# Kernel optimization log

Measured on AMD Instinct MI355X. Metric: run time of the kernel, lower is better.

## Reference

```python
import jax, jax.numpy as jnp
import numpy as np
import math

B, N, DIM = 16, 1024, 384
DEPTH, HEADS, DH = 6, 6, 64
INNER = HEADS * DH          # 384
MLP = 1536
LN_EPS = 1e-5


def setup_inputs() -> dict:
    key = jax.random.key(0)
    ks = jax.random.split(key, 7)
    s = 0.02
    x = jax.random.normal(ks[0], (B, N, DIM), dtype=jnp.float32)
    ln1_g = jnp.ones((DEPTH, DIM), jnp.float32)
    ln1_b = jnp.zeros((DEPTH, DIM), jnp.float32)
    qkv_w = jax.random.normal(ks[1], (DEPTH, DIM, 3 * INNER), jnp.float32) * s
    temp = jnp.full((DEPTH,), math.log(DH ** -0.5), jnp.float32)
    out_w = jax.random.normal(ks[2], (DEPTH, INNER, DIM), jnp.float32) * s
    out_b = jnp.zeros((DEPTH, DIM), jnp.float32)
    ln2_g = jnp.ones((DEPTH, DIM), jnp.float32)
    ln2_b = jnp.zeros((DEPTH, DIM), jnp.float32)
    ff_w1 = jax.random.normal(ks[3], (DEPTH, DIM, MLP), jnp.float32) * s
    ff_b1 = jnp.zeros((DEPTH, MLP), jnp.float32)
    ff_w2 = jax.random.normal(ks[4], (DEPTH, MLP, DIM), jnp.float32) * s
    ff_b2 = jnp.zeros((DEPTH, DIM), jnp.float32)
    return dict(x=x, ln1_g=ln1_g, ln1_b=ln1_b, qkv_w=qkv_w, temp=temp,
                out_w=out_w, out_b=out_b, ln2_g=ln2_g, ln2_b=ln2_b,
                ff_w1=ff_w1, ff_b1=ff_b1, ff_w2=ff_w2, ff_b2=ff_b2)


def _ln(x, g, b):
    m = jnp.mean(x, axis=-1, keepdims=True)
    v = jnp.var(x, axis=-1, keepdims=True)
    return (x - m) * jax.lax.rsqrt(v + LN_EPS) * g + b


def reference(x, ln1_g, ln1_b, qkv_w, temp, out_w, out_b,
              ln2_g, ln2_b, ff_w1, ff_b1, ff_w2, ff_b2):
    neg = -jnp.finfo(x.dtype).max
    eye = jnp.eye(N, dtype=bool)

    def step(x, p):
        g1, b1, wqkv, t, wo, bo, g2, b2, w1, bb1, w2, bb2 = p
        # --- PreNorm + LSA attention ---
        h = _ln(x, g1, b1)
        qkv = h @ wqkv                              # [B, N, 3*INNER]
        q, k, v = jnp.split(qkv, 3, axis=-1)
        split_heads = lambda a: a.reshape(B, N, HEADS, DH).transpose(0, 2, 1, 3)
        q, k, v = split_heads(q), split_heads(k), split_heads(v)
        dots = jnp.einsum('bhnd,bhmd->bhnm', q, k) * jnp.exp(t)
        dots = jnp.where(eye, neg, dots)            # mask diagonal (LSA)
        attn = jax.nn.softmax(dots, axis=-1)
        o = jnp.einsum('bhnm,bhmd->bhnd', attn, v)
        o = o.transpose(0, 2, 1, 3).reshape(B, N, INNER)
        x = x + o @ wo + bo
        # --- PreNorm + FeedForward (exact GELU) ---
        h2 = _ln(x, g2, b2)
        ff = jax.nn.gelu(h2 @ w1 + bb1, approximate=False) @ w2 + bb2
        x = x + ff
        return x, None

    params = (ln1_g, ln1_b, qkv_w, temp, out_w, out_b,
              ln2_g, ln2_b, ff_w1, ff_b1, ff_w2, ff_b2)
    x, _ = jax.lax.scan(step, x, params)
    return x
```

## Files before the change

### kernel.cpp

```cpp
#include <hip/hip_runtime.h>
#include <hip/hip_bf16.h>
#include <math.h>

#define B_     16
#define NTOK   1024
#define DIM_   384
#define DEPTH_ 6
#define HEADS_ 6
#define DH_    64
#define MLP_   1536
#define MTOT   (B_ * NTOK)
#define NBH    (B_ * HEADS_)

typedef unsigned short u16;
typedef unsigned int u32;
typedef short short8 __attribute__((ext_vector_type(8)));
typedef float f32x4 __attribute__((ext_vector_type(4)));

static __device__ __forceinline__ u16 f2b(float f) {
    __hip_bfloat16 h = __float2bfloat16(f);
    return *reinterpret_cast<u16*>(&h);
}

#define GLOAD_LDS16(gp, lp)                                                     \
    __builtin_amdgcn_global_load_lds(                                           \
        (const __attribute__((address_space(1))) void*)(gp),                    \
        (__attribute__((address_space(3))) void*)(lp), 16, 0, 0)

__launch_bounds__(256)
__global__ void transpose_w_kernel(const float* __restrict__ W, u16* __restrict__ WT,
                                   int K, int N) {
    const int layer = blockIdx.z;
    W  += (size_t)layer * K * N;
    WT += (size_t)layer * K * N;
    __shared__ u16 tile[64 * 72];
    const int t = threadIdx.x;
    const int k0 = blockIdx.x * 64, n0 = blockIdx.y * 64;
    const int row = t >> 2, cs = (t & 3) * 16;
    const float4* src = reinterpret_cast<const float4*>(W + (size_t)(k0 + row) * N + n0 + cs);
#pragma unroll
    for (int i = 0; i < 4; i++) {
        float4 f = src[i];
        tile[row * 72 + cs + i * 4 + 0] = f2b(f.x);
        tile[row * 72 + cs + i * 4 + 1] = f2b(f.y);
        tile[row * 72 + cs + i * 4 + 2] = f2b(f.z);
        tile[row * 72 + cs + i * 4 + 3] = f2b(f.w);
    }
    __syncthreads();
    const int nrow = row, ks = cs;
    u16 vals[16] __attribute__((aligned(16)));
#pragma unroll
    for (int e = 0; e < 16; e++) vals[e] = tile[(ks + e) * 72 + nrow];
    u16* dst = WT + (size_t)(n0 + nrow) * K + k0 + ks;
    *reinterpret_cast<short8*>(dst)     = *reinterpret_cast<short8*>(&vals[0]);
    *reinterpret_cast<short8*>(dst + 8) = *reinterpret_cast<short8*>(&vals[8]);
}

__launch_bounds__(256)
__global__ void ln_kernel(const float* __restrict__ x, const float* __restrict__ g,
                          const float* __restrict__ b, u16* __restrict__ h) {
    const int tok  = blockIdx.x * 4 + (threadIdx.x >> 6);
    const int lane = threadIdx.x & 63;
    const float* xr = x + (size_t)tok * DIM_;
    float v[6];
    float s = 0.f;
#pragma unroll
    for (int i = 0; i < 6; i++) { v[i] = xr[lane + i * 64]; s += v[i]; }
#pragma unroll
    for (int m = 1; m < 64; m <<= 1) s += __shfl_xor(s, m);
    const float mean = s * (1.f / 384.f);
    float qs = 0.f;
#pragma unroll
    for (int i = 0; i < 6; i++) { float d = v[i] - mean; qs += d * d; }
#pragma unroll
    for (int m = 1; m < 64; m <<= 1) qs += __shfl_xor(qs, m);
    const float inv = rsqrtf(qs * (1.f / 384.f) + 1e-5f);
    u16* hr = h + (size_t)tok * DIM_;
#pragma unroll
    for (int i = 0; i < 6; i++) {
        const int c = lane + i * 64;
        hr[c] = f2b((v[i] - mean) * inv * g[c] + b[c]);
    }
}

enum { EPI_QKV = 0, EPI_RES = 1, EPI_GELU = 2 };

template <int EPI>
__launch_bounds__(256)
__global__ void gemm_kernel(const u16* __restrict__ A, const u16* __restrict__ BT, int K,
                            const float* __restrict__ bias, const float* __restrict__ resid,
                            float* __restrict__ outf, u16* __restrict__ outb, int ldc,
                            u16* __restrict__ qkv_base) {
    __shared__ u16 As[128 * 32];
    __shared__ u16 Bs[128 * 32];
    const int t = threadIdx.x;
    const int lane = t & 63, w = t >> 6;
    const int wm = w >> 1, wn = w & 1;
    const int m0 = blockIdx.x * 128, n0 = blockIdx.y * 128;

    f32x4 acc[4][4] = {};

    const int c0 = w * 2, c1 = w * 2 + 1;
    const int seg = (lane & 3) * 8;
    const u16* agp0 = A  + (size_t)(m0 + c0 * 16 + (lane >> 2)) * K + seg;
    const u16* agp1 = A  + (size_t)(m0 + c1 * 16 + (lane >> 2)) * K + seg;
    const u16* bgp0 = BT + (size_t)(n0 + c0 * 16 + (lane >> 2)) * K + seg;
    const u16* bgp1 = BT + (size_t)(n0 + c1 * 16 + (lane >> 2)) * K + seg;
    u16* asl0 = &As[c0 * 512];
    u16* asl1 = &As[c1 * 512];
    u16* bsl0 = &Bs[c0 * 512];
    u16* bsl1 = &Bs[c1 * 512];

    for (int kk = 0; kk < K; kk += 32) {
        __syncthreads();
        GLOAD_LDS16(agp0 + kk, asl0);
        GLOAD_LDS16(agp1 + kk, asl1);
        GLOAD_LDS16(bgp0 + kk, bsl0);
        GLOAD_LDS16(bgp1 + kk, bsl1);
        __syncthreads();
        short8 af[4], bf[4];
#pragma unroll
        for (int i = 0; i < 4; i++)
            af[i] = *reinterpret_cast<const short8*>(
                &As[(wm * 64 + i * 16 + (lane & 15)) * 32 + (lane >> 4) * 8]);
#pragma unroll
        for (int j = 0; j < 4; j++)
            bf[j] = *reinterpret_cast<const short8*>(
                &Bs[(wn * 64 + j * 16 + (lane & 15)) * 32 + (lane >> 4) * 8]);
#pragma unroll
        for (int i = 0; i < 4; i++)
#pragma unroll
            for (int j = 0; j < 4; j++)
                acc[i][j] = __builtin_amdgcn_mfma_f32_16x16x32_bf16(af[i], bf[j], acc[i][j], 0, 0, 0);
    }

    const int rbase = (lane >> 4) * 4;
    const int cb = lane & 15;
#pragma unroll
    for (int i = 0; i < 4; i++) {
#pragma unroll
        for (int j = 0; j < 4; j++) {
#pragma unroll
            for (int r = 0; r < 4; r++) {
                const int m = m0 + wm * 64 + i * 16 + rbase + r;
                const int c = n0 + wn * 64 + j * 16 + cb;
                const float val = acc[i][j][r];
                if constexpr (EPI == EPI_QKV) {
                    const int which = c / 384;
                    const int cc = c - which * 384;
                    const int head = cc >> 6, dh = cc & 63;
                    const int b = m >> 10, n = m & 1023;
                    qkv_base[(size_t)which * ((size_t)NBH * NTOK * DH_) +
                             ((size_t)((b * HEADS_ + head) * NTOK + n)) * DH_ + dh] = f2b(val);
                } else if constexpr (EPI == EPI_RES) {
                    outf[(size_t)m * ldc + c] = resid[(size_t)m * ldc + c] + bias[c] + val;
                } else {
                    const float xg = val + bias[c];
                    const float ge = 0.5f * xg * (1.0f + erff(xg * 0.70710678118f));
                    outb[(size_t)m * ldc + c] = f2b(ge);
                }
            }
        }
    }
}

__launch_bounds__(256)
__global__ void attn_kernel(const u16* __restrict__ q, const u16* __restrict__ k,
                            const u16* __restrict__ v, const float* __restrict__ temp,
                            u16* __restrict__ o) {
    __shared__ u16 Ks[64 * 72];
    __shared__ u16 Vt[64 * 88];
    __shared__ u16 Ps[4][16 * 80];
    const int t = threadIdx.x, lane = t & 63, w = t >> 6;
    const int g8 = lane >> 4, qi = lane & 15;
    const int bh = blockIdx.x, q0 = blockIdx.y * 64;
    const float scale = __expf(temp[0]);
    const size_t base = (size_t)bh * (NTOK * DH_);

    short8 bq[2];
#pragma unroll
    for (int s = 0; s < 2; s++)
        bq[s] = *reinterpret_cast<const short8*>(
            &q[base + (size_t)(q0 + w * 16 + qi) * 64 + s * 32 + g8 * 8]);

    float m_s = -3.0e38f, l_s = 0.f;
    f32x4 accO[4] = {};
    const int qglob = q0 + w * 16 + qi;

    for (int j0 = 0; j0 < NTOK; j0 += 64) {
        __syncthreads();
#pragma unroll
        for (int cc = 0; cc < 2; cc++) {
            const int idx = t + cc * 256;
            const int row = idx >> 3, ch = idx & 7;
            *reinterpret_cast<short8*>(&Ks[row * 72 + ch * 8]) =
                *reinterpret_cast<const short8*>(&k[base + (size_t)(j0 + row) * 64 + ch * 8]);
        }
#pragma unroll
        for (int cc = 0; cc < 2; cc++) {
            const int kv0 = w * 16 + cc * 8;
            u16 tmp[8] __attribute__((aligned(16)));
#pragma unroll
            for (int j = 0; j < 8; j++)
                tmp[j] = v[base + (size_t)(j0 + kv0 + j) * 64 + lane];
            *reinterpret_cast<short8*>(&Vt[lane * 88 + kv0]) = *reinterpret_cast<short8*>(&tmp[0]);
        }
        __syncthreads();

        f32x4 sf[4] = {};
#pragma unroll
        for (int c = 0; c < 4; c++)
#pragma unroll
            for (int s = 0; s < 2; s++) {
                short8 af = *reinterpret_cast<const short8*>(
                    &Ks[(c * 16 + qi) * 72 + s * 32 + g8 * 8]);
                sf[c] = __builtin_amdgcn_mfma_f32_16x16x32_bf16(af, bq[s], sf[c], 0, 0, 0);
            }

        float p[4][4];
        float vmax = -3.0e38f;
#pragma unroll
        for (int c = 0; c < 4; c++)
#pragma unroll
            for (int r = 0; r < 4; r++) {
                float sv = sf[c][r] * scale;
                const int kvg = j0 + c * 16 + g8 * 4 + r;
                if (kvg == qglob) sv = -1.0e30f;
                p[c][r] = sv;
                vmax = fmaxf(vmax, sv);
            }
        vmax = fmaxf(vmax, __shfl_xor(vmax, 16));
        vmax = fmaxf(vmax, __shfl_xor(vmax, 32));
        const float mnew = fmaxf(m_s, vmax);
        const float alpha = __expf(m_s - mnew);
        m_s = mnew;
        float tsum = 0.f;
#pragma unroll
        for (int c = 0; c < 4; c++)
#pragma unroll
            for (int r = 0; r < 4; r++) {
                const float pe = __expf(p[c][r] - mnew);
                p[c][r] = pe;
                tsum += pe;
            }
        tsum += __shfl_xor(tsum, 16);
        tsum += __shfl_xor(tsum, 32);
        l_s = l_s * alpha + tsum;

#pragma unroll
        for (int r = 0; r < 4; r++) {
            const float a_r = __shfl(alpha, g8 * 4 + r, 64);
#pragma unroll
            for (int g = 0; g < 4; g++) accO[g][r] *= a_r;
        }

#pragma unroll
        for (int c = 0; c < 4; c++) {
            u32 lo = (u32)f2b(p[c][0]) | ((u32)f2b(p[c][1]) << 16);
            u32 hi = (u32)f2b(p[c][2]) | ((u32)f2b(p[c][3]) << 16);
            uint2 pr; pr.x = lo; pr.y = hi;
            *reinterpret_cast<uint2*>(&Ps[w][qi * 80 + c * 16 + g8 * 4]) = pr;
        }

#pragma unroll
        for (int s = 0; s < 2; s++) {
            short8 ap = *reinterpret_cast<const short8*>(&Ps[w][qi * 80 + s * 32 + g8 * 8]);
#pragma unroll
            for (int g = 0; g < 4; g++) {
                short8 bv = *reinterpret_cast<const short8*>(
                    &Vt[(g * 16 + qi) * 88 + s * 32 + g8 * 8]);
                accO[g] = __builtin_amdgcn_mfma_f32_16x16x32_bf16(ap, bv, accO[g], 0, 0, 0);
            }
        }
    }

    const int bidx = bh / HEADS_, head = bh % HEADS_;
#pragma unroll
    for (int r = 0; r < 4; r++) {
        const float li = __shfl(l_s, g8 * 4 + r, 64);
        const float linv = 1.f / li;
        const int n = q0 + w * 16 + g8 * 4 + r;
#pragma unroll
        for (int g = 0; g < 4; g++) {
            const int dh = g * 16 + qi;
            o[((size_t)(bidx * NTOK + n)) * DIM_ + head * DH_ + dh] = f2b(accO[g][r] * linv);
        }
    }
}

extern "C" void kernel_launch(void* const* d_in, const int* in_sizes, int n_in,
                              void* d_out, int out_size, void* d_ws, size_t ws_size,
                              hipStream_t stream) {
    const float* x_in  = (const float*)d_in[0];
    const float* ln1_g = (const float*)d_in[1];
    const float* ln1_b = (const float*)d_in[2];
    const float* qkv_w = (const float*)d_in[3];
    const float* temp  = (const float*)d_in[4];
    const float* out_w = (const float*)d_in[5];
    const float* out_b = (const float*)d_in[6];
    const float* ln2_g = (const float*)d_in[7];
    const float* ln2_b = (const float*)d_in[8];
    const float* ff_w1 = (const float*)d_in[9];
    const float* ff_b1 = (const float*)d_in[10];
    const float* ff_w2 = (const float*)d_in[11];
    const float* ff_b2 = (const float*)d_in[12];

    char* ws = (char*)d_ws;
    size_t off = 0;
    auto alloc = [&](size_t bytes) -> void* {
        void* p = ws + off;
        off += (bytes + 255) & ~(size_t)255;
        return p;
    };
    u16* wt_qkv = (u16*)alloc((size_t)DEPTH_ * 1152 * 384 * 2);
    u16* wt_out = (u16*)alloc((size_t)DEPTH_ * 384 * 384 * 2);
    u16* wt_ff1 = (u16*)alloc((size_t)DEPTH_ * 1536 * 384 * 2);
    u16* wt_ff2 = (u16*)alloc((size_t)DEPTH_ * 384 * 1536 * 2);
    u16* H      = (u16*)alloc((size_t)MTOT * DIM_ * 2);
    u16* QKV    = (u16*)alloc((size_t)MTOT * MLP_ * 2);
    u16* MID    = QKV;

    float* X = (float*)d_out;

    hipMemcpyAsync(X, x_in, (size_t)MTOT * DIM_ * sizeof(float),
                   hipMemcpyDeviceToDevice, stream);

    transpose_w_kernel<<<dim3(6, 18, DEPTH_), 256, 0, stream>>>(qkv_w, wt_qkv, 384, 1152);
    transpose_w_kernel<<<dim3(6, 6, DEPTH_), 256, 0, stream>>>(out_w, wt_out, 384, 384);
    transpose_w_kernel<<<dim3(6, 24, DEPTH_), 256, 0, stream>>>(ff_w1, wt_ff1, 384, 1536);
    transpose_w_kernel<<<dim3(24, 6, DEPTH_), 256, 0, stream>>>(ff_w2, wt_ff2, 1536, 384);

    const size_t qkv_plane = (size_t)NBH * NTOK * DH_;

    for (int layer = 0; layer < DEPTH_; layer++) {
        ln_kernel<<<4096, 256, 0, stream>>>(X, ln1_g + layer * DIM_, ln1_b + layer * DIM_, H);
        gemm_kernel<EPI_QKV><<<dim3(128, 9), 256, 0, stream>>>(
            H, wt_qkv + (size_t)layer * 1152 * 384, 384,
            nullptr, nullptr, nullptr, nullptr, 0, QKV);
        attn_kernel<<<dim3(96, 16), 256, 0, stream>>>(
            QKV, QKV + qkv_plane, QKV + 2 * qkv_plane, temp + layer, H);
        gemm_kernel<EPI_RES><<<dim3(128, 3), 256, 0, stream>>>(
            H, wt_out + (size_t)layer * 384 * 384, 384,
            out_b + layer * DIM_, X, X, nullptr, DIM_, nullptr);
        ln_kernel<<<4096, 256, 0, stream>>>(X, ln2_g + layer * DIM_, ln2_b + layer * DIM_, H);
        gemm_kernel<EPI_GELU><<<dim3(128, 12), 256, 0, stream>>>(
            H, wt_ff1 + (size_t)layer * 1536 * 384, 384,
            ff_b1 + layer * MLP_, nullptr, nullptr, MID, MLP_, nullptr);
        gemm_kernel<EPI_RES><<<dim3(128, 3), 256, 0, stream>>>(
            MID, wt_ff2 + (size_t)layer * 384 * 1536, 1536,
            ff_b2 + layer * DIM_, X, X, nullptr, DIM_, nullptr);
    }
}
```

Baseline: 1.399 ms.

## Pre-swizzle K and pre-transpose V in QKV epilogue; async LDS loads in attention

The QKV GEMM epilogue now writes K with an XOR-swizzled column order and V already transposed and swizzled, so attention can fill LDS with direct global-to-LDS 16-byte loads. This removes the strided per-element V transpose and the padded shared arrays. The softmax also moves to exp2 with a prescaled log2e factor, checks the diagonal mask only on the diagonal tile, and rescales the running max lazily, only when the new max exceeds the old by more than a threshold. The QKV epilogue's scattered 2-byte stores for K and the transposed V layout may cost extra write efficiency.

```diff
diff --git a/kernel.cpp b/kernel.cpp
--- a/kernel.cpp
+++ b/kernel.cpp
@@ -11,6 +11,7 @@
 #define MLP_   1536
 #define MTOT   (B_ * NTOK)
 #define NBH    (B_ * HEADS_)
+#define QKV_PLANE ((size_t)NBH * NTOK * DH_)
 
 typedef unsigned short u16;
 typedef unsigned int u32;
@@ -140,24 +141,48 @@
     for (int i = 0; i < 4; i++) {
 #pragma unroll
         for (int j = 0; j < 4; j++) {
-#pragma unroll
-            for (int r = 0; r < 4; r++) {
-                const int m = m0 + wm * 64 + i * 16 + rbase + r;
+            if constexpr (EPI == EPI_QKV) {
                 const int c = n0 + wn * 64 + j * 16 + cb;
-                const float val = acc[i][j][r];
-                if constexpr (EPI == EPI_QKV) {
-                    const int which = c / 384;
-                    const int cc = c - which * 384;
-                    const int head = cc >> 6, dh = cc & 63;
-                    const int b = m >> 10, n = m & 1023;
-                    qkv_base[(size_t)which * ((size_t)NBH * NTOK * DH_) +
-                             ((size_t)((b * HEADS_ + head) * NTOK + n)) * DH_ + dh] = f2b(val);
-                } else if constexpr (EPI == EPI_RES) {
-                    outf[(size_t)m * ldc + c] = resid[(size_t)m * ldc + c] + bias[c] + val;
+                const int which = c / 384;
+                const int cc = c - which * 384;
+                const int head = cc >> 6, dh = cc & 63;
+                const int nb = m0 + wm * 64 + i * 16 + rbase;
+                const int b = nb >> 10, nt = nb & 1023;
+                const size_t bh = (size_t)(b * HEADS_ + head);
+                if (which == 2) {
+                    u16 pk[4] __attribute__((aligned(8)));
+#pragma unroll
+                    for (int r = 0; r < 4; r++) pk[r] = f2b(acc[i][j][r]);
+                    const int nsw = (nt & ~63) | ((((nt >> 3) & 7) ^ (dh & 7)) << 3) | (nt & 7);
+                    *reinterpret_cast<uint2*>(
+                        &qkv_base[2 * QKV_PLANE + bh * 65536 + (size_t)dh * 1024 + nsw]) =
+                        *reinterpret_cast<uint2*>(pk);
+                } else if (which == 1) {
+#pragma unroll
+                    for (int r = 0; r < 4; r++) {
+                        const int n = nt + r;
+                        const int dsw = (((dh >> 3) ^ (n & 7)) << 3) | (dh & 7);
+                        qkv_base[QKV_PLANE + bh * 65536 + (size_t)n * 64 + dsw] =
+                            f2b(acc[i][j][r]);
+                    }
                 } else {
-                    const float xg = val + bias[c];
-                    const float ge = 0.5f * xg * (1.0f + erff(xg * 0.70710678118f));
-                    outb[(size_t)m * ldc + c] = f2b(ge);
+#pragma unroll
+                    for (int r = 0; r < 4; r++)
+                        qkv_base[bh * 65536 + (size_t)(nt + r) * 64 + dh] = f2b(acc[i][j][r]);
+                }
+            } else {
+#pragma unroll
+                for (int r = 0; r < 4; r++) {
+                    const int m = m0 + wm * 64 + i * 16 + rbase + r;
+                    const int c = n0 + wn * 64 + j * 16 + cb;
+                    const float val = acc[i][j][r];
+                    if constexpr (EPI == EPI_RES) {
+                        outf[(size_t)m * ldc + c] = resid[(size_t)m * ldc + c] + bias[c] + val;
+                    } else {
+                        const float xg = val + bias[c];
+                        const float ge = 0.5f * xg * (1.0f + erff(xg * 0.70710678118f));
+                        outb[(size_t)m * ldc + c] = f2b(ge);
+                    }
                 }
             }
         }
@@ -168,13 +193,13 @@
 __global__ void attn_kernel(const u16* __restrict__ q, const u16* __restrict__ k,
                             const u16* __restrict__ v, const float* __restrict__ temp,
                             u16* __restrict__ o) {
-    __shared__ u16 Ks[64 * 72];
-    __shared__ u16 Vt[64 * 88];
+    __shared__ u16 Kt[64 * 64];
+    __shared__ u16 Vt[64 * 64];
     __shared__ u16 Ps[4][16 * 80];
     const int t = threadIdx.x, lane = t & 63, w = t >> 6;
     const int g8 = lane >> 4, qi = lane & 15;
     const int bh = blockIdx.x, q0 = blockIdx.y * 64;
-    const float scale = __expf(temp[0]);
+    const float scale2 = __expf(temp[0]) * 1.4426950408889634f;
     const size_t base = (size_t)bh * (NTOK * DH_);
 
     short8 bq[2];
@@ -187,72 +212,83 @@
     f32x4 accO[4] = {};
     const int qglob = q0 + w * 16 + qi;
 
+    const int srow = w * 8 + (lane >> 3);
+    const int schunk = (lane & 7) * 8;
+    const u16* kg0 = k + base + (size_t)srow * 64 + schunk;
+    const u16* vg0 = v + base + (size_t)srow * 1024 + schunk;
+    u16* klds = &Kt[w * 512];
+    u16* vlds = &Vt[w * 512];
+
     for (int j0 = 0; j0 < NTOK; j0 += 64) {
         __syncthreads();
-#pragma unroll
-        for (int cc = 0; cc < 2; cc++) {
-            const int idx = t + cc * 256;
-            const int row = idx >> 3, ch = idx & 7;
-            *reinterpret_cast<short8*>(&Ks[row * 72 + ch * 8]) =
-                *reinterpret_cast<const short8*>(&k[base + (size_t)(j0 + row) * 64 + ch * 8]);
-        }
-#pragma unroll
-        for (int cc = 0; cc < 2; cc++) {
-            const int kv0 = w * 16 + cc * 8;
-            u16 tmp[8] __attribute__((aligned(16)));
-#pragma unroll
-            for (int j = 0; j < 8; j++)
-                tmp[j] = v[base + (size_t)(j0 + kv0 + j) * 64 + lane];
-            *reinterpret_cast<short8*>(&Vt[lane * 88 + kv0]) = *reinterpret_cast<short8*>(&tmp[0]);
-        }
+        GLOAD_LDS16(kg0 + (size_t)j0 * 64,            klds);
+        GLOAD_LDS16(kg0 + (size_t)j0 * 64 + 32 * 64,  klds + 2048);
+        GLOAD_LDS16(vg0 + j0,                         vlds);
+        GLOAD_LDS16(vg0 + j0 + 32 * 1024,             vlds + 2048);
         __syncthreads();
 
         f32x4 sf[4] = {};
 #pragma unroll
-        for (int c = 0; c < 4; c++)
+        for (int c = 0; c < 4; c++) {
+            const int krow = c * 16 + qi;
 #pragma unroll
             for (int s = 0; s < 2; s++) {
                 short8 af = *reinterpret_cast<const short8*>(
-                    &Ks[(c * 16 + qi) * 72 + s * 32 + g8 * 8]);
+                    &Kt[krow * 64 + (((s * 4 + g8) ^ (krow & 7)) << 3)]);
                 sf[c] = __builtin_amdgcn_mfma_f32_16x16x32_bf16(af, bq[s], sf[c], 0, 0, 0);
             }
+        }
 
         float p[4][4];
         float vmax = -3.0e38f;
-#pragma unroll
-        for (int c = 0; c < 4; c++)
-#pragma unroll
-            for (int r = 0; r < 4; r++) {
-                float sv = sf[c][r] * scale;
-                const int kvg = j0 + c * 16 + g8 * 4 + r;
-                if (kvg == qglob) sv = -1.0e30f;
-                p[c][r] = sv;
-                vmax = fmaxf(vmax, sv);
-            }
+        if (j0 == q0) {
+#pragma unroll
+            for (int c = 0; c < 4; c++)
+#pragma unroll
+                for (int r = 0; r < 4; r++) {
+                    float sv = sf[c][r] * scale2;
+                    if (j0 + c * 16 + g8 * 4 + r == qglob) sv = -3.0e37f;
+                    p[c][r] = sv;
+                    vmax = fmaxf(vmax, sv);
+                }
+        } else {
+#pragma unroll
+            for (int c = 0; c < 4; c++)
+#pragma unroll
+                for (int r = 0; r < 4; r++) {
+                    const float sv = sf[c][r] * scale2;
+                    p[c][r] = sv;
+                    vmax = fmaxf(vmax, sv);
+                }
+        }
         vmax = fmaxf(vmax, __shfl_xor(vmax, 16));
         vmax = fmaxf(vmax, __shfl_xor(vmax, 32));
-        const float mnew = fmaxf(m_s, vmax);
-        const float alpha = __expf(m_s - mnew);
-        m_s = mnew;
+
+        if (!__all(vmax - m_s <= 11.0f)) {
+            const float mnew = fmaxf(m_s, vmax);
+            const float alpha = exp2f(m_s - mnew);
+            m_s = mnew;
+            l_s *= alpha;
+#pragma unroll
+            for (int r = 0; r < 4; r++) {
+                const float a_r = __shfl(alpha, g8 * 4 + r, 64);
+#pragma unroll
+                for (int g = 0; g < 4; g++) accO[g][r] *= a_r;
+            }
+        }
+
         float tsum = 0.f;
 #pragma unroll
         for (int c = 0; c < 4; c++)
 #pragma unroll
             for (int r = 0; r < 4; r++) {
-                const float pe = __expf(p[c][r] - mnew);
+                const float pe = exp2f(p[c][r] - m_s);
                 p[c][r] = pe;
                 tsum += pe;
             }
         tsum += __shfl_xor(tsum, 16);
         tsum += __shfl_xor(tsum, 32);
-        l_s = l_s * alpha + tsum;
-
-#pragma unroll
-        for (int r = 0; r < 4; r++) {
-            const float a_r = __shfl(alpha, g8 * 4 + r, 64);
-#pragma unroll
-            for (int g = 0; g < 4; g++) accO[g][r] *= a_r;
-        }
+        l_s += tsum;
 
 #pragma unroll
         for (int c = 0; c < 4; c++) {
@@ -267,8 +303,9 @@
             short8 ap = *reinterpret_cast<const short8*>(&Ps[w][qi * 80 + s * 32 + g8 * 8]);
 #pragma unroll
             for (int g = 0; g < 4; g++) {
+                const int vrow = g * 16 + qi;
                 short8 bv = *reinterpret_cast<const short8*>(
-                    &Vt[(g * 16 + qi) * 88 + s * 32 + g8 * 8]);
+                    &Vt[vrow * 64 + (((s * 4 + g8) ^ (vrow & 7)) << 3)]);
                 accO[g] = __builtin_amdgcn_mfma_f32_16x16x32_bf16(ap, bv, accO[g], 0, 0, 0);
             }
         }
@@ -330,15 +367,13 @@
     transpose_w_kernel<<<dim3(6, 24, DEPTH_), 256, 0, stream>>>(ff_w1, wt_ff1, 384, 1536);
     transpose_w_kernel<<<dim3(24, 6, DEPTH_), 256, 0, stream>>>(ff_w2, wt_ff2, 1536, 384);
 
-    const size_t qkv_plane = (size_t)NBH * NTOK * DH_;
-
     for (int layer = 0; layer < DEPTH_; layer++) {
         ln_kernel<<<4096, 256, 0, stream>>>(X, ln1_g + layer * DIM_, ln1_b + layer * DIM_, H);
         gemm_kernel<EPI_QKV><<<dim3(128, 9), 256, 0, stream>>>(
             H, wt_qkv + (size_t)layer * 1152 * 384, 384,
             nullptr, nullptr, nullptr, nullptr, 0, QKV);
         attn_kernel<<<dim3(96, 16), 256, 0, stream>>>(
-            QKV, QKV + qkv_plane, QKV + 2 * qkv_plane, temp + layer, H);
+            QKV, QKV + QKV_PLANE, QKV + 2 * QKV_PLANE, temp + layer, H);
         gemm_kernel<EPI_RES><<<dim3(128, 3), 256, 0, stream>>>(
             H, wt_out + (size_t)layer * 384 * 384, 384,
             out_b + layer * DIM_, X, X, nullptr, DIM_, nullptr);
```

Result: no change. 1.388 ms (-0.8%).
